# Kernel optimization log

Measured on AMD Instinct MI355X. Metric: run time of the kernel, lower is better.

## Reference

```python
import jax, jax.numpy as jnp
import numpy as np

N_SEND = 49152   # 12 * 64^2 HEALPix nodes
N_REC = 65536    # 256x256 receiver grid
N_EDGES = 262144 # N_REC * 4 nearest senders
D_MODEL = 256
EDGE_IN, EDGE_OUT = 4, 64
LIN_IN, LIN_OUT = 320, 256
B = 2


def setup_inputs() -> dict:
    key = jax.random.key(0)
    ks = jax.random.split(key, 8)
    x = jax.random.normal(ks[0], (B, N_SEND, D_MODEL), dtype=jnp.float32)
    senders = jax.random.randint(ks[1], (N_EDGES,), 0, N_SEND, dtype=jnp.int32)
    receivers = jax.random.randint(ks[2], (N_EDGES,), 0, N_REC, dtype=jnp.int32)
    edge_index = jnp.stack([senders, receivers], axis=0)
    edge_attr = jax.random.normal(ks[3], (N_EDGES, EDGE_IN), dtype=jnp.float32)
    s = lambda fan_in: 1.0 / np.sqrt(fan_in)
    return {
        "x": x,
        "edge_index": edge_index,
        "edge_attr": edge_attr,
        "ee_w1": jax.random.normal(ks[4], (EDGE_IN, EDGE_OUT), dtype=jnp.float32) * s(EDGE_IN),
        "ee_b1": jnp.zeros((EDGE_OUT,), dtype=jnp.float32),
        "ee_w2": jax.random.normal(ks[5], (EDGE_OUT, EDGE_OUT), dtype=jnp.float32) * s(EDGE_OUT),
        "ee_b2": jnp.zeros((EDGE_OUT,), dtype=jnp.float32),
        "ff_w1": jax.random.normal(ks[6], (LIN_IN, LIN_OUT), dtype=jnp.float32) * s(LIN_IN),
        "ff_b1": jnp.zeros((LIN_OUT,), dtype=jnp.float32),
        "ff_w2": jax.random.normal(ks[7], (LIN_OUT, LIN_OUT), dtype=jnp.float32) * s(LIN_OUT),
        "ff_b2": jnp.zeros((LIN_OUT,), dtype=jnp.float32),
    }


def reference(x, edge_index, edge_attr,
              ee_w1, ee_b1, ee_w2, ee_b2,
              ff_w1, ff_b1, ff_w2, ff_b2):
    senders, receivers = edge_index[0], edge_index[1]
    # edge embedder MLP: [E, edge_in] -> [E, edge_out]
    h = jax.nn.relu(edge_attr @ ee_w1 + ee_b1)
    edge_feat = h @ ee_w2 + ee_b2                       # [E, edge_out]
    # gather sender node features: [B, E, d_model]
    v_s = x[:, senders, :]
    # concat with broadcast edge features: [B, E, d_model + edge_out]
    ef = jnp.broadcast_to(edge_feat[None], (x.shape[0],) + edge_feat.shape)
    v_s_prime = jnp.concatenate([v_s, ef], axis=-1)
    # scatter-sum onto receiver nodes: [B, n_rec, lin_in]
    v_m_sum = jnp.zeros((x.shape[0], N_REC, v_s_prime.shape[-1]), dtype=x.dtype)
    v_m_sum = v_m_sum.at[:, receivers, :].add(v_s_prime)
    # g2m feedforward: [B, n_rec, lin_out]
    h2 = jax.nn.relu(v_m_sum @ ff_w1 + ff_b1)
    return h2 @ ff_w2 + ff_b2
```

## Files before the change

### kernel.cpp

```cpp
#include <hip/hip_runtime.h>
#include <hip/hip_bf16.h>

#define N_SEND 49152
#define N_REC  65536
#define N_EDGES 262144
#define D_MODEL 256
#define EDGE_IN 4
#define EDGE_OUT 64
#define LIN_IN 320
#define LIN_OUT 256
#define BATCH 2

#define GBM 64

typedef __attribute__((ext_vector_type(4))) float f32x4;
typedef __attribute__((ext_vector_type(8))) short bf16x8;

static __device__ __forceinline__ unsigned short f2bf(float f) {
    union { float f; unsigned u; } v; v.f = f;
    unsigned r = v.u + 0x7FFF + ((v.u >> 16) & 1);
    return (unsigned short)(r >> 16);
}
static __device__ __forceinline__ float bf2f(unsigned short h) {
    union { unsigned u; float f; } v; v.u = ((unsigned)h) << 16; return v.f;
}

static __device__ __forceinline__ void async_copy16(void* lds_ptr, const void* g_ptr) {
    __builtin_amdgcn_global_load_lds(
        (const __attribute__((address_space(1))) void*)g_ptr,
        (__attribute__((address_space(3))) void*)lds_ptr, 16, 0, 0);
}

__global__ __launch_bounds__(256) void wprep(
    const float* __restrict__ w1, const float* __restrict__ w2,
    const float* __restrict__ ew2,
    unsigned short* __restrict__ w1t, unsigned short* __restrict__ w2t,
    unsigned short* __restrict__ w2et)
{
    const int tid = blockIdx.x * 256 + threadIdx.x;
    if (tid < 256 * LIN_IN) {
        const int n = tid / LIN_IN, k = tid - n * LIN_IN;
        w1t[tid] = f2bf(w1[k * LIN_OUT + n]);
    } else if (tid < 256 * LIN_IN + 256 * LIN_OUT) {
        const int t2 = tid - 256 * LIN_IN;
        const int n = t2 >> 8, k = t2 & 255;
        w2t[t2] = f2bf(w2[k * LIN_OUT + n]);
    } else if (tid < 256 * LIN_IN + 256 * LIN_OUT + EDGE_OUT * EDGE_OUT) {
        const int t3 = tid - (256 * LIN_IN + 256 * LIN_OUT);
        const int n = t3 >> 6, k = t3 & 63;
        w2et[t3] = f2bf(ew2[k * EDGE_OUT + n]);
    }
}

__global__ __launch_bounds__(256) void prep_fused(
    const float* __restrict__ x, unsigned short* __restrict__ xb, int nconv,
    const int* __restrict__ receivers, const float* __restrict__ edge_attr,
    const float* __restrict__ ee_w1, const float* __restrict__ ee_b1,
    const unsigned short* __restrict__ w2et, const float* __restrict__ ee_b2,
    unsigned short* __restrict__ efs, int* __restrict__ counts)
{
    __shared__ __align__(16) unsigned short h_lds[256 * EDGE_OUT];

    const int bid = blockIdx.x;
    const int tid = threadIdx.x;

    if (bid < nconv) {
        const size_t i = ((size_t)bid * 256 + tid) * 8;
        const float4 v0 = *(const float4*)&x[i];
        const float4 v1 = *(const float4*)&x[i + 4];
        bf16x8 o;
        o[0] = (short)f2bf(v0.x); o[1] = (short)f2bf(v0.y);
        o[2] = (short)f2bf(v0.z); o[3] = (short)f2bf(v0.w);
        o[4] = (short)f2bf(v1.x); o[5] = (short)f2bf(v1.y);
        o[6] = (short)f2bf(v1.z); o[7] = (short)f2bf(v1.w);
        *(bf16x8*)&xb[i] = o;
        return;
    }
    const int b2 = bid - nconv;

    {
        const int e0 = b2 * 256;
        atomicAdd(&counts[receivers[e0 + tid]], 1);

        {
            const float4 ea = *(const float4*)&edge_attr[(size_t)(e0 + tid) * EDGE_IN];
#pragma unroll
            for (int kb = 0; kb < 8; ++kb) {
                bf16x8 hv;
#pragma unroll
                for (int j = 0; j < 8; ++j) {
                    const int k = kb * 8 + j;
                    float a = ee_b1[k];
                    a += ea.x * ee_w1[0 * EDGE_OUT + k];
                    a += ea.y * ee_w1[1 * EDGE_OUT + k];
                    a += ea.z * ee_w1[2 * EDGE_OUT + k];
                    a += ea.w * ee_w1[3 * EDGE_OUT + k];
                    hv[j] = (short)f2bf(fmaxf(a, 0.0f));
                }
                *(bf16x8*)&h_lds[tid * EDGE_OUT + ((kb ^ (tid & 7)) * 8)] = hv;
            }
        }

        const int lane = tid & 63, wave = tid >> 6;
        const int n16 = lane & 15, hi = lane >> 4;

        bf16x8 bfr[2][4];
#pragma unroll
        for (int ch = 0; ch < 2; ++ch)
#pragma unroll
            for (int c = 0; c < 4; ++c)
                bfr[ch][c] = *(const bf16x8*)&w2et[(size_t)(16 * c + n16) * EDGE_OUT + ch * 32 + hi * 8];

        f32x4 acc[4][4];
#pragma unroll
        for (int c = 0; c < 4; ++c) {
            const float bv = ee_b2[16 * c + n16];
#pragma unroll
            for (int t = 0; t < 4; ++t) {
                acc[t][c][0] = bv; acc[t][c][1] = bv; acc[t][c][2] = bv; acc[t][c][3] = bv;
            }
        }

#pragma unroll
        for (int ch = 0; ch < 2; ++ch) {
            bf16x8 af[4];
#pragma unroll
            for (int t = 0; t < 4; ++t) {
                const int row = 64 * wave + 16 * t + n16;
                const int slot = (4 * ch + hi) ^ (row & 7);
                af[t] = *(const bf16x8*)&h_lds[row * EDGE_OUT + slot * 8];
            }
#pragma unroll
            for (int c = 0; c < 4; ++c)
#pragma unroll
                for (int t = 0; t < 4; ++t)
                    acc[t][c] = __builtin_amdgcn_mfma_f32_16x16x32_bf16(af[t], bfr[ch][c], acc[t][c], 0, 0, 0);
        }

#pragma unroll
        for (int t = 0; t < 4; ++t)
#pragma unroll
            for (int c = 0; c < 4; ++c)
#pragma unroll
                for (int r = 0; r < 4; ++r)
                    efs[(size_t)(e0 + 64 * wave + 16 * t + 4 * hi + r) * EDGE_OUT + 16 * c + n16] =
                        f2bf(acc[t][c][r]);
    }
}

__global__ __launch_bounds__(1024) void scan_kernel(
    const int* __restrict__ counts, int* __restrict__ row_ptr,
    int* __restrict__ cursor)
{
    __shared__ int sums[1024];
    const int t = threadIdx.x;
    const int4* c4 = (const int4*)(counts + t * 64);

    int s = 0;
#pragma unroll
    for (int i = 0; i < 16; ++i) { const int4 c = c4[i]; s += c.x + c.y + c.z + c.w; }
    sums[t] = s;
    __syncthreads();

    for (int off = 1; off < 1024; off <<= 1) {
        const int v = (t >= off) ? sums[t - off] : 0;
        __syncthreads();
        sums[t] += v;
        __syncthreads();
    }

    int run = sums[t] - s;
#pragma unroll
    for (int i = 0; i < 16; ++i) {
        const int4 c = c4[i];
        int4 w;
        w.x = run; w.y = run + c.x; w.z = w.y + c.y; w.w = w.z + c.z;
        run = w.w + c.w;
        ((int4*)(row_ptr + t * 64))[i] = w;
        ((int4*)(cursor + t * 64))[i] = w;
    }
    if (t == 1023) row_ptr[N_REC] = run;
}

__global__ __launch_bounds__(256) void fill_kernel(
    const int* __restrict__ senders, const int* __restrict__ receivers,
    int* __restrict__ cursor, int2* __restrict__ eord2)
{
    const int e = blockIdx.x * 256 + threadIdx.x;
    const int r = receivers[e];
    const int pos = atomicAdd(&cursor[r], 1);
    eord2[pos] = make_int2(e, senders[e]);
}

__global__ __launch_bounds__(256) void gather_kernel(
    const unsigned short* __restrict__ xb,
    const unsigned short* __restrict__ efs,
    const int* __restrict__ row_ptr,
    const int2* __restrict__ eord2,
    unsigned short* __restrict__ vmb)
{
    const int lane = threadIdx.x & 63;
    const int wave = threadIdx.x >> 6;
    const int r = blockIdx.x * 4 + wave;
    const int beg = row_ptr[r], end = row_ptr[r + 1];
    const int half = lane >> 5, l2 = lane & 31;
    const size_t xbase = (size_t)half * N_SEND * D_MODEL;

    float ax[8] = {0, 0, 0, 0, 0, 0, 0, 0};
    float ae[8] = {0, 0, 0, 0, 0, 0, 0, 0};

    for (int chunk = beg; chunk < end; chunk += 64) {
        const int n = min(64, end - chunk);
        int myidx = 0, myeidx = 0;
        if (chunk + lane < end) {
            const int2 p2 = eord2[chunk + lane];
            myeidx = p2.x; myidx = p2.y;
        }
        for (int i = 0; i < n; i += 4) {
            bf16x8 vx[4], ve[4];
#pragma unroll
            for (int u = 0; u < 4; ++u) {
                const int s = __shfl(myidx, i + u);
                const int e = __shfl(myeidx, i + u);
                const bool p = (i + u < n);
                const bf16x8 z = {0, 0, 0, 0, 0, 0, 0, 0};
                vx[u] = z; ve[u] = z;
                if (p) vx[u] = *(const bf16x8*)&xb[xbase + (size_t)s * D_MODEL + l2 * 8];
                if (p && lane < 8) ve[u] = *(const bf16x8*)&efs[(size_t)e * EDGE_OUT + lane * 8];
            }
#pragma unroll
            for (int u = 0; u < 4; ++u)
#pragma unroll
                for (int j = 0; j < 8; ++j)
                    ax[j] += bf2f((unsigned short)vx[u][j]);
            if (lane < 8) {
#pragma unroll
                for (int u = 0; u < 4; ++u)
#pragma unroll
                    for (int j = 0; j < 8; ++j)
                        ae[j] += bf2f((unsigned short)ve[u][j]);
            }
        }
    }

    bf16x8 o;
#pragma unroll
    for (int j = 0; j < 8; ++j) o[j] = (short)f2bf(ax[j]);
    *(bf16x8*)&vmb[((size_t)(half * N_REC + r)) * LIN_IN + l2 * 8] = o;
    if (lane < 8) {
        bf16x8 oe;
#pragma unroll
        for (int j = 0; j < 8; ++j) oe[j] = (short)f2bf(ae[j]);
        *(bf16x8*)&vmb[((size_t)r) * LIN_IN + D_MODEL + lane * 8] = oe;
        *(bf16x8*)&vmb[((size_t)(N_REC + r)) * LIN_IN + D_MODEL + lane * 8] = oe;
    }
}

__global__ __launch_bounds__(256, 2) void node_mlp_fused(
    const unsigned short* __restrict__ vmb,
    const unsigned short* __restrict__ w1t,
    const float* __restrict__ b1,
    const unsigned short* __restrict__ w2t,
    const float* __restrict__ b2,
    float* __restrict__ out)
{
    __shared__ __align__(16) char lds[73728];

    const int tid  = threadIdx.x;
    const int lane = tid & 63, wc = tid >> 6;
    const int n16  = lane & 15, hi = lane >> 4;
    const size_t row0 = (size_t)blockIdx.x * GBM;
    char* const wB = lds + 40960 + wc * 8192;

    const int f_l = (n16 & 3) ^ ((n16 >> 2) & 3);
    const int hsl = (hi ^ f_l) << 4;

    auto stageA = [&](int kc) {
        const int row = tid >> 2;
        const int sl = (tid & 3) ^ ((row & 3) ^ ((row >> 2) & 3));
        const unsigned short* g = vmb + (row0 + row) * LIN_IN + kc * 32 + sl * 8;
        char* l = lds + (kc << 12) + ((tid >> 6) << 10);
        async_copy16(l, g);
    };
    auto issueB = [&](const unsigned short* BT, int ldk, int kk, int buf) {
#pragma unroll
        for (int p = 0; p < 4; ++p) {
            const int i = p * 64 + lane;
            const int row = i >> 2;
            const int sl = (i & 3) ^ ((row & 3) ^ ((row >> 2) & 3));
            const unsigned short* g = BT + (size_t)(64 * wc + row) * ldk + kk + sl * 8;
            char* l = wB + (buf << 12) + (p << 10);
            async_copy16(l, g);
        }
    };

#pragma unroll
    for (int kc = 0; kc < LIN_IN / 32; ++kc) stageA(kc);
    issueB(w1t, LIN_IN, 0, 0);
    __syncthreads();

    f32x4 acc[4][4];
#pragma unroll
    for (int c = 0; c < 4; ++c) {
        const float bv = b1[64 * wc + 16 * c + n16];
#pragma unroll
        for (int t = 0; t < 4; ++t) {
            acc[t][c][0] = bv; acc[t][c][1] = bv; acc[t][c][2] = bv; acc[t][c][3] = bv;
        }
    }

    int buf = 0;
    for (int step = 0; step < LIN_IN / 32; ++step) {
        if (step + 1 < LIN_IN / 32) {
            issueB(w1t, LIN_IN, (step + 1) * 32, buf ^ 1);
            __builtin_amdgcn_sched_barrier(0);
            asm volatile("s_waitcnt vmcnt(4)" ::: "memory");
        } else {
            asm volatile("s_waitcnt vmcnt(0)" ::: "memory");
        }
        __builtin_amdgcn_sched_barrier(0);

        bf16x8 af[4], bf[4];
        const char* Ab = lds + (step << 12);
        const char* Bb = wB + (buf << 12);
#pragma unroll
        for (int t = 0; t < 4; ++t)
            af[t] = *(const bf16x8*)(Ab + (16 * t + n16) * 64 + hsl);
#pragma unroll
        for (int c = 0; c < 4; ++c)
            bf[c] = *(const bf16x8*)(Bb + (16 * c + n16) * 64 + hsl);
#pragma unroll
        for (int c = 0; c < 4; ++c)
#pragma unroll
            for (int t = 0; t < 4; ++t)
                acc[t][c] = __builtin_amdgcn_mfma_f32_16x16x32_bf16(af[t], bf[c], acc[t][c], 0, 0, 0);
        buf ^= 1;
    }

    __syncthreads();

    issueB(w2t, LIN_OUT, 0, 0);

#pragma unroll
    for (int t = 0; t < 4; ++t)
#pragma unroll
        for (int c = 0; c < 4; ++c) {
            const int col = 64 * wc + 16 * c + n16;
            const int kc = col >> 5;
            const int b  = (col & 31) * 2;
            const int gslot = b >> 4;
#pragma unroll
            for (int r = 0; r < 4; ++r) {
                const int lrow = 16 * t + 4 * hi + r;
                const int f = (lrow & 3) ^ ((lrow >> 2) & 3);
                *(unsigned short*)(lds + (kc << 12) + lrow * 64 + (((gslot ^ f) << 4) | (b & 15))) =
                    f2bf(fmaxf(acc[t][c][r], 0.0f));
            }
        }
    asm volatile("s_waitcnt lgkmcnt(0)" ::: "memory");
    __builtin_amdgcn_s_barrier();
    __builtin_amdgcn_sched_barrier(0);

    f32x4 acc2[4][4];
#pragma unroll
    for (int c = 0; c < 4; ++c) {
        const float bv = b2[64 * wc + 16 * c + n16];
#pragma unroll
        for (int t = 0; t < 4; ++t) {
            acc2[t][c][0] = bv; acc2[t][c][1] = bv; acc2[t][c][2] = bv; acc2[t][c][3] = bv;
        }
    }

    buf = 0;
    for (int step = 0; step < LIN_OUT / 32; ++step) {
        if (step + 1 < LIN_OUT / 32) {
            issueB(w2t, LIN_OUT, (step + 1) * 32, buf ^ 1);
            __builtin_amdgcn_sched_barrier(0);
            asm volatile("s_waitcnt vmcnt(4)" ::: "memory");
        } else {
            asm volatile("s_waitcnt vmcnt(0)" ::: "memory");
        }
        __builtin_amdgcn_sched_barrier(0);

        bf16x8 af[4], bf[4];
        const char* Hb = lds + (step << 12);
        const char* Bb = wB + (buf << 12);
#pragma unroll
        for (int t = 0; t < 4; ++t)
            af[t] = *(const bf16x8*)(Hb + (16 * t + n16) * 64 + hsl);
#pragma unroll
        for (int c = 0; c < 4; ++c)
            bf[c] = *(const bf16x8*)(Bb + (16 * c + n16) * 64 + hsl);
#pragma unroll
        for (int c = 0; c < 4; ++c)
#pragma unroll
            for (int t = 0; t < 4; ++t)
                acc2[t][c] = __builtin_amdgcn_mfma_f32_16x16x32_bf16(af[t], bf[c], acc2[t][c], 0, 0, 0);
        buf ^= 1;
    }

#pragma unroll
    for (int t = 0; t < 4; ++t)
#pragma unroll
        for (int c = 0; c < 4; ++c)
#pragma unroll
            for (int r = 0; r < 4; ++r)
                out[(row0 + 16 * t + 4 * hi + r) * LIN_OUT + 64 * wc + 16 * c + n16] =
                    acc2[t][c][r];
}

extern "C" void kernel_launch(void* const* d_in, const int* in_sizes, int n_in,
                              void* d_out, int out_size, void* d_ws, size_t ws_size,
                              hipStream_t stream) {
    const float* x         = (const float*)d_in[0];
    const int*   edge_idx  = (const int*)d_in[1];
    const float* edge_attr = (const float*)d_in[2];
    const float* ee_w1     = (const float*)d_in[3];
    const float* ee_b1     = (const float*)d_in[4];
    const float* ee_w2     = (const float*)d_in[5];
    const float* ee_b2     = (const float*)d_in[6];
    const float* ff_w1     = (const float*)d_in[7];
    const float* ff_b1     = (const float*)d_in[8];
    const float* ff_w2     = (const float*)d_in[9];
    const float* ff_b2     = (const float*)d_in[10];
    float* out = (float*)d_out;

    const int* senders   = edge_idx;
    const int* receivers = edge_idx + N_EDGES;

    char* ws = (char*)d_ws;
    size_t off = 0;
    auto alloc = [&](size_t bytes) { char* p = ws + off; off += (bytes + 511) & ~511ull; return p; };

    unsigned short* vmb = (unsigned short*)alloc((size_t)BATCH * N_REC * LIN_IN * 2);
    unsigned short* efs = (unsigned short*)alloc((size_t)N_EDGES * EDGE_OUT * 2);
    unsigned short* xb  = (unsigned short*)alloc((size_t)BATCH * N_SEND * D_MODEL * 2);
    unsigned short* w1t = (unsigned short*)alloc((size_t)256 * LIN_IN * 2);
    unsigned short* w2t = (unsigned short*)alloc((size_t)256 * LIN_OUT * 2);
    unsigned short* w2et = (unsigned short*)alloc((size_t)EDGE_OUT * EDGE_OUT * 2);
    int* row_ptr        = (int*)alloc((size_t)(N_REC + 1) * 4);
    int* counts         = (int*)alloc((size_t)N_REC * 4);
    int* cursor         = (int*)alloc((size_t)N_REC * 4);
    int2* eord2         = (int2*)alloc((size_t)N_EDGES * 8);

    hipMemsetAsync(counts, 0, (size_t)N_REC * 4, stream);

    const int wprep_elems = 256 * LIN_IN + 256 * LIN_OUT + EDGE_OUT * EDGE_OUT;
    wprep<<<(wprep_elems + 255) / 256, 256, 0, stream>>>(
        ff_w1, ff_w2, ee_w2, w1t, w2t, w2et);

    const int nconv = (int)((size_t)BATCH * N_SEND * D_MODEL / 8 / 256);
    prep_fused<<<nconv + N_EDGES / 256, 256, 0, stream>>>(
        x, xb, nconv, receivers, edge_attr, ee_w1, ee_b1, w2et, ee_b2, efs, counts);

    scan_kernel<<<1, 1024, 0, stream>>>(counts, row_ptr, cursor);

    fill_kernel<<<N_EDGES / 256, 256, 0, stream>>>(
        senders, receivers, cursor, eord2);

    gather_kernel<<<N_REC / 4, 256, 0, stream>>>(
        xb, efs, row_ptr, eord2, vmb);

    node_mlp_fused<<<(BATCH * N_REC) / GBM, 256, 0, stream>>>(
        vmb, w1t, ff_b1, w2t, ff_b2, out);
}
```

Measured before the change: 234.8 us.

## Reorder preprocessing to merge histogram with weight prep and fill with edge MLP

Moves the receiver histogram into the weight-preparation kernel so the scan can run before the large x-conversion and edge-MLP kernel. The CSR fill step then runs as extra blocks inside that kernel, which removes one kernel launch and lets the fill overlap with the bf16 conversion and the edge embedding. The cost is a heavier first kernel and one more grid of atomic blocks mixed in with the compute blocks.

New measurement: 236.3 us. Within noise of the previous version (+0.7%).

```diff
diff --git a/kernel.cpp b/kernel.cpp
--- a/kernel.cpp
+++ b/kernel.cpp
@@ -31,33 +31,78 @@
         (__attribute__((address_space(3))) void*)lds_ptr, 16, 0, 0);
 }
 
-__global__ __launch_bounds__(256) void wprep(
+#define WPREP_BLKS ((256 * LIN_IN + 256 * LIN_OUT + EDGE_OUT * EDGE_OUT + 255) / 256)
+
+__global__ __launch_bounds__(256) void wprep_hist(
     const float* __restrict__ w1, const float* __restrict__ w2,
     const float* __restrict__ ew2,
     unsigned short* __restrict__ w1t, unsigned short* __restrict__ w2t,
-    unsigned short* __restrict__ w2et)
+    unsigned short* __restrict__ w2et,
+    const int* __restrict__ receivers, int* __restrict__ counts)
 {
-    const int tid = blockIdx.x * 256 + threadIdx.x;
-    if (tid < 256 * LIN_IN) {
-        const int n = tid / LIN_IN, k = tid - n * LIN_IN;
-        w1t[tid] = f2bf(w1[k * LIN_OUT + n]);
-    } else if (tid < 256 * LIN_IN + 256 * LIN_OUT) {
-        const int t2 = tid - 256 * LIN_IN;
-        const int n = t2 >> 8, k = t2 & 255;
-        w2t[t2] = f2bf(w2[k * LIN_OUT + n]);
-    } else if (tid < 256 * LIN_IN + 256 * LIN_OUT + EDGE_OUT * EDGE_OUT) {
-        const int t3 = tid - (256 * LIN_IN + 256 * LIN_OUT);
-        const int n = t3 >> 6, k = t3 & 63;
-        w2et[t3] = f2bf(ew2[k * EDGE_OUT + n]);
-    }
-}
-
-__global__ __launch_bounds__(256) void prep_fused(
+    const int bid = blockIdx.x;
+    if (bid < WPREP_BLKS) {
+        const int tid = bid * 256 + threadIdx.x;
+        if (tid < 256 * LIN_IN) {
+            const int n = tid / LIN_IN, k = tid - n * LIN_IN;
+            w1t[tid] = f2bf(w1[k * LIN_OUT + n]);
+        } else if (tid < 256 * LIN_IN + 256 * LIN_OUT) {
+            const int t2 = tid - 256 * LIN_IN;
+            const int n = t2 >> 8, k = t2 & 255;
+            w2t[t2] = f2bf(w2[k * LIN_OUT + n]);
+        } else if (tid < 256 * LIN_IN + 256 * LIN_OUT + EDGE_OUT * EDGE_OUT) {
+            const int t3 = tid - (256 * LIN_IN + 256 * LIN_OUT);
+            const int n = t3 >> 6, k = t3 & 63;
+            w2et[t3] = f2bf(ew2[k * EDGE_OUT + n]);
+        }
+        return;
+    }
+    const int e = (bid - WPREP_BLKS) * 256 + threadIdx.x;
+    atomicAdd(&counts[receivers[e]], 1);
+}
+
+__global__ __launch_bounds__(1024) void scan_kernel(
+    const int* __restrict__ counts, int* __restrict__ row_ptr,
+    int* __restrict__ cursor)
+{
+    __shared__ int sums[1024];
+    const int t = threadIdx.x;
+    const int4* c4 = (const int4*)(counts + t * 64);
+
+    int s = 0;
+#pragma unroll
+    for (int i = 0; i < 16; ++i) { const int4 c = c4[i]; s += c.x + c.y + c.z + c.w; }
+    sums[t] = s;
+    __syncthreads();
+
+    for (int off = 1; off < 1024; off <<= 1) {
+        const int v = (t >= off) ? sums[t - off] : 0;
+        __syncthreads();
+        sums[t] += v;
+        __syncthreads();
+    }
+
+    int run = sums[t] - s;
+#pragma unroll
+    for (int i = 0; i < 16; ++i) {
+        const int4 c = c4[i];
+        int4 w;
+        w.x = run; w.y = run + c.x; w.z = w.y + c.y; w.w = w.z + c.z;
+        run = w.w + c.w;
+        ((int4*)(row_ptr + t * 64))[i] = w;
+        ((int4*)(cursor + t * 64))[i] = w;
+    }
+    if (t == 1023) row_ptr[N_REC] = run;
+}
+
+__global__ __launch_bounds__(256) void prep_fill(
     const float* __restrict__ x, unsigned short* __restrict__ xb, int nconv,
-    const int* __restrict__ receivers, const float* __restrict__ edge_attr,
+    const int* __restrict__ senders, const int* __restrict__ receivers,
+    const float* __restrict__ edge_attr,
     const float* __restrict__ ee_w1, const float* __restrict__ ee_b1,
     const unsigned short* __restrict__ w2et, const float* __restrict__ ee_b2,
-    unsigned short* __restrict__ efs, int* __restrict__ counts)
+    unsigned short* __restrict__ efs,
+    int* __restrict__ cursor, int2* __restrict__ eord2)
 {
     __shared__ __align__(16) unsigned short h_lds[256 * EDGE_OUT];
 
@@ -78,9 +123,8 @@
     }
     const int b2 = bid - nconv;
 
-    {
+    if (b2 < N_EDGES / 256) {
         const int e0 = b2 * 256;
-        atomicAdd(&counts[receivers[e0 + tid]], 1);
 
         {
             const float4 ea = *(const float4*)&edge_attr[(size_t)(e0 + tid) * EDGE_IN];
@@ -145,51 +189,15 @@
                 for (int r = 0; r < 4; ++r)
                     efs[(size_t)(e0 + 64 * wave + 16 * t + 4 * hi + r) * EDGE_OUT + 16 * c + n16] =
                         f2bf(acc[t][c][r]);
-    }
-}
-
-__global__ __launch_bounds__(1024) void scan_kernel(
-    const int* __restrict__ counts, int* __restrict__ row_ptr,
-    int* __restrict__ cursor)
-{
-    __shared__ int sums[1024];
-    const int t = threadIdx.x;
-    const int4* c4 = (const int4*)(counts + t * 64);
-
-    int s = 0;
-#pragma unroll
-    for (int i = 0; i < 16; ++i) { const int4 c = c4[i]; s += c.x + c.y + c.z + c.w; }
-    sums[t] = s;
-    __syncthreads();
-
-    for (int off = 1; off < 1024; off <<= 1) {
-        const int v = (t >= off) ? sums[t - off] : 0;
-        __syncthreads();
-        sums[t] += v;
-        __syncthreads();
-    }
-
-    int run = sums[t] - s;
-#pragma unroll
-    for (int i = 0; i < 16; ++i) {
-        const int4 c = c4[i];
-        int4 w;
-        w.x = run; w.y = run + c.x; w.z = w.y + c.y; w.w = w.z + c.z;
-        run = w.w + c.w;
-        ((int4*)(row_ptr + t * 64))[i] = w;
-        ((int4*)(cursor + t * 64))[i] = w;
-    }
-    if (t == 1023) row_ptr[N_REC] = run;
-}
-
-__global__ __launch_bounds__(256) void fill_kernel(
-    const int* __restrict__ senders, const int* __restrict__ receivers,
-    int* __restrict__ cursor, int2* __restrict__ eord2)
-{
-    const int e = blockIdx.x * 256 + threadIdx.x;
-    const int r = receivers[e];
-    const int pos = atomicAdd(&cursor[r], 1);
-    eord2[pos] = make_int2(e, senders[e]);
+        return;
+    }
+
+    {
+        const int e = (b2 - N_EDGES / 256) * 256 + tid;
+        const int r = receivers[e];
+        const int pos = atomicAdd(&cursor[r], 1);
+        eord2[pos] = make_int2(e, senders[e]);
+    }
 }
 
 __global__ __launch_bounds__(256) void gather_kernel(
@@ -445,18 +453,15 @@
 
     hipMemsetAsync(counts, 0, (size_t)N_REC * 4, stream);
 
-    const int wprep_elems = 256 * LIN_IN + 256 * LIN_OUT + EDGE_OUT * EDGE_OUT;
-    wprep<<<(wprep_elems + 255) / 256, 256, 0, stream>>>(
-        ff_w1, ff_w2, ee_w2, w1t, w2t, w2et);
+    wprep_hist<<<WPREP_BLKS + N_EDGES / 256, 256, 0, stream>>>(
+        ff_w1, ff_w2, ee_w2, w1t, w2t, w2et, receivers, counts);
+
+    scan_kernel<<<1, 1024, 0, stream>>>(counts, row_ptr, cursor);
 
     const int nconv = (int)((size_t)BATCH * N_SEND * D_MODEL / 8 / 256);
-    prep_fused<<<nconv + N_EDGES / 256, 256, 0, stream>>>(
-        x, xb, nconv, receivers, edge_attr, ee_w1, ee_b1, w2et, ee_b2, efs, counts);
-
-    scan_kernel<<<1, 1024, 0, stream>>>(counts, row_ptr, cursor);
-
-    fill_kernel<<<N_EDGES / 256, 256, 0, stream>>>(
-        senders, receivers, cursor, eord2);
+    prep_fill<<<nconv + N_EDGES / 256 + N_EDGES / 256, 256, 0, stream>>>(
+        x, xb, nconv, senders, receivers, edge_attr, ee_w1, ee_b1, w2et, ee_b2,
+        efs, cursor, eord2);
 
     gather_kernel<<<N_REC / 4, 256, 0, stream>>>(
         xb, efs, row_ptr, eord2, vmb);
```
